# Performance work log

Measured on AMD Instinct MI355X. Metric: run time of the kernel, lower is better.

## Reference

```python
import jax, jax.numpy as jnp
import numpy as np

N = 50000      # nodes
E = 400000     # edges (before self-loops)
IN = 128
HID = 64
HEADS = 8
OUT = 3
NEG_SLOPE = 0.2
EPS = 1e-6


def setup_inputs() -> dict:
    key = jax.random.key(0)
    ks = jax.random.split(key, 32)
    def nrm(k, shape, s=0.05):
        return jax.random.normal(k, shape, dtype=jnp.float32) * s
    inp = {}
    inp['x'] = nrm(ks[0], (N, IN), 1.0)
    inp['edge_index'] = jax.random.randint(ks[1], (2, E), 0, N)
    inp['res_W'] = nrm(ks[2], (OUT, IN))
    inp['res_b'] = jnp.zeros((OUT,), jnp.float32)
    # (in, out, heads, concat) per GAT layer
    dims = [(IN, HID, HEADS, True), (HID * HEADS, HID, HEADS, True),
            (HID * HEADS, HID, HEADS, True), (HID * HEADS, OUT, 1, False)]
    j = 3
    for i, (ci, co, h, cc) in enumerate(dims):
        inp['ln_g%d' % i] = jnp.ones((ci,), jnp.float32)
        inp['ln_b%d' % i] = jnp.zeros((ci,), jnp.float32)
        inp['W%d' % i] = nrm(ks[j], (h * co, ci)); j += 1
        inp['asr%d' % i] = nrm(ks[j], (h, co)); j += 1
        inp['adt%d' % i] = nrm(ks[j], (h, co)); j += 1
        inp['b%d' % i] = jnp.zeros((h * co if cc else co,), jnp.float32)
    return inp


def layer_norm(x, g, b):
    mu = x.mean(-1, keepdims=True)
    var = ((x - mu) ** 2).mean(-1, keepdims=True)
    return (x - mu) / jnp.sqrt(var + EPS) * g + b


def gat_conv(x, src, dst, W, a_src, a_dst, bias, heads, co, concat):
    n = x.shape[0]
    h = (x @ W.T).reshape(n, heads, co)                    # [N,H,C]
    al_src = jnp.sum(h * a_src, axis=-1)                   # [N,H]
    al_dst = jnp.sum(h * a_dst, axis=-1)                   # [N,H]
    e = jax.nn.leaky_relu(al_src[src] + al_dst[dst], NEG_SLOPE)  # [E',H]
    # segment softmax over incoming edges of each destination node
    m = jax.ops.segment_max(e, dst, num_segments=n)
    e = jnp.exp(e - m[dst])
    s = jax.ops.segment_sum(e, dst, num_segments=n)
    alpha = e / s[dst]                                     # [E',H]
    msg = h[src] * alpha[..., None]                        # [E',H,C]
    out = jax.ops.segment_sum(msg, dst, num_segments=n)    # [N,H,C]
    out = out.reshape(n, heads * co) if concat else out.mean(axis=1)
    return out + bias


def reference(x, edge_index, res_W, res_b,
              ln_g0, ln_b0, W0, asr0, adt0, b0,
              ln_g1, ln_b1, W1, asr1, adt1, b1,
              ln_g2, ln_b2, W2, asr2, adt2, b2,
              ln_g3, ln_b3, W3, asr3, adt3, b3):
    n = x.shape[0]
    loops = jnp.arange(n)
    src = jnp.concatenate([edge_index[0], loops])          # add self-loops (PyG default)
    dst = jnp.concatenate([edge_index[1], loops])
    residual = x @ res_W.T + res_b
    layers = [(ln_g0, ln_b0, W0, asr0, adt0, b0, HEADS, HID, True),
              (ln_g1, ln_b1, W1, asr1, adt1, b1, HEADS, HID, True),
              (ln_g2, ln_b2, W2, asr2, adt2, b2, HEADS, HID, True),
              (ln_g3, ln_b3, W3, asr3, adt3, b3, 1, OUT, False)]
    h = x
    num_layers = len(layers)
    for i, (g, bb, W, a_s, a_d, bi, hd, co, cc) in enumerate(layers):
        x_res = h
        h = layer_norm(h, g, bb)
        h = gat_conv(h, src, dst, W, a_s, a_d, bi, hd, co, cc)
        if i < num_layers - 1:
            h = jax.nn.gelu(h, approximate=False)
            if h.shape == x_res.shape:
                h = h + x_res
    return h + residual
```

## Files before the change

### kernel.cpp

```cpp
#include <hip/hip_runtime.h>
#include <math.h>

#define NN 50000
#define MPAD 50048
#define EE 400000
#define NE 450000
#define IN_F 128
#define NEG_SLOPE 0.2f
#define EPSV 1e-6f

typedef unsigned short bf16u;
typedef short bf8_t __attribute__((ext_vector_type(8)));
typedef float f32x4 __attribute__((ext_vector_type(4)));

__device__ __forceinline__ float bf2f(unsigned int u) {
    return __uint_as_float(u << 16);
}
__device__ __forceinline__ float bf2f_hi(unsigned int u) {
    return __uint_as_float(u & 0xFFFF0000u);
}
__device__ __forceinline__ bf16u f2bf(float f) {
    unsigned int u = __float_as_uint(f);
    unsigned int r = (u + 0x7FFFu + ((u >> 16) & 1u)) >> 16;
    return (bf16u)r;
}
__device__ __forceinline__ float gelu_f(float v) {
    return 0.5f * v * (1.0f + erff(v * 0.70710678118654752f));
}
__device__ __forceinline__ float lrelu(float v) {
    return fmaxf(v, NEG_SLOPE * v);
}
__device__ __forceinline__ void fma8(float* acc, float a, uint4 u) {
    acc[0] = fmaf(a, bf2f(u.x & 0xFFFFu), acc[0]);
    acc[1] = fmaf(a, bf2f_hi(u.x),        acc[1]);
    acc[2] = fmaf(a, bf2f(u.y & 0xFFFFu), acc[2]);
    acc[3] = fmaf(a, bf2f_hi(u.y),        acc[3]);
    acc[4] = fmaf(a, bf2f(u.z & 0xFFFFu), acc[4]);
    acc[5] = fmaf(a, bf2f_hi(u.z),        acc[5]);
    acc[6] = fmaf(a, bf2f(u.w & 0xFFFFu), acc[6]);
    acc[7] = fmaf(a, bf2f_hi(u.w),        acc[7]);
}

__device__ __forceinline__ void gload_lds16(const void* g, void* l) {
    __builtin_amdgcn_global_load_lds(
        (__attribute__((address_space(1))) void*)(g),
        (__attribute__((address_space(3))) void*)(l), 16, 0, 0);
}

__global__ void k_zero_i32(int* p, int n) {
    int i = blockIdx.x * 256 + threadIdx.x;
    if (i < n) p[i] = 0;
}

__global__ void k_deg(const int* __restrict__ ei, int* __restrict__ deg) {
    int i = blockIdx.x * 256 + threadIdx.x;
    if (i >= NE) return;
    int d = (i < EE) ? ei[EE + i] : (i - EE);
    atomicAdd(&deg[d], 1);
}

__global__ __launch_bounds__(256) void k_scan1(const int* __restrict__ deg,
                                               int* __restrict__ incl,
                                               int* __restrict__ bsums, int n) {
    __shared__ int sm[1024];
    int base = blockIdx.x * 1024;
    for (int i = threadIdx.x; i < 1024; i += 256)
        sm[i] = (base + i < n) ? deg[base + i] : 0;
    __syncthreads();
    for (int off = 1; off < 1024; off <<= 1) {
        int v[4];
#pragma unroll
        for (int j = 0; j < 4; j++) {
            int i = threadIdx.x + 256 * j;
            v[j] = (i >= off) ? sm[i - off] : 0;
        }
        __syncthreads();
#pragma unroll
        for (int j = 0; j < 4; j++) {
            int i = threadIdx.x + 256 * j;
            sm[i] += v[j];
        }
        __syncthreads();
    }
    for (int i = threadIdx.x; i < 1024; i += 256)
        if (base + i < n) incl[base + i] = sm[i];
    if (threadIdx.x == 0) bsums[blockIdx.x] = sm[1023];
}

__global__ void k_scan2(int* bsums, int nb) {
    if (threadIdx.x == 0 && blockIdx.x == 0) {
        int run = 0;
        for (int i = 0; i < nb; i++) { int v = bsums[i]; bsums[i] = run; run += v; }
    }
}

__global__ void k_scan3(const int* __restrict__ deg, int* __restrict__ rowptr,
                        int* __restrict__ cursor, const int* __restrict__ bsums,
                        int n, int ne) {
    int i = blockIdx.x * 256 + threadIdx.x;
    if (i < n) {
        int excl = rowptr[i] + bsums[i >> 10] - deg[i];
        rowptr[i] = excl;
        cursor[i] = excl;
    }
    if (i == n) rowptr[n] = ne;
}

__global__ void k_scatter(const int* __restrict__ ei, int* __restrict__ cursor,
                          int* __restrict__ col) {
    int i = blockIdx.x * 256 + threadIdx.x;
    if (i >= NE) return;
    int s, d;
    if (i < EE) { s = ei[i]; d = ei[EE + i]; }
    else        { s = i - EE; d = i - EE; }
    int p = atomicAdd(&cursor[d], 1);
    col[p] = s;
}

__global__ void k_cast3(const float* __restrict__ w0, bf16u* __restrict__ o0,
                        const float* __restrict__ w1, bf16u* __restrict__ o1,
                        const float* __restrict__ w2, bf16u* __restrict__ o2) {
    int i = blockIdx.x * 256 + threadIdx.x;
    if (i < 65536) { o0[i] = f2bf(w0[i]); return; }
    i -= 65536;
    if (i < 262144) { o1[i] = f2bf(w1[i]); return; }
    i -= 262144;
    if (i < 262144) o2[i] = f2bf(w2[i]);
}

__global__ __launch_bounds__(256) void k_castres2(const float* __restrict__ x,
                                                  const float* __restrict__ rw,
                                                  const float* __restrict__ rb,
                                                  const float* __restrict__ g0,
                                                  const float* __restrict__ b0,
                                                  bf16u* __restrict__ abuf,
                                                  float* __restrict__ res, int n) {
    int row = (blockIdx.x * 256 + threadIdx.x) >> 6;
    int lane = threadIdx.x & 63;
    if (row >= n) return;
    float2 v = *(const float2*)(x + (size_t)row * 128 + lane * 2);
    float2 w0 = *(const float2*)(rw + 0 * 128 + lane * 2);
    float2 w1 = *(const float2*)(rw + 1 * 128 + lane * 2);
    float2 w2 = *(const float2*)(rw + 2 * 128 + lane * 2);
    float s = v.x + v.y, s2 = v.x * v.x + v.y * v.y;
    float a0 = v.x * w0.x + v.y * w0.y;
    float a1 = v.x * w1.x + v.y * w1.y;
    float a2 = v.x * w2.x + v.y * w2.y;
#pragma unroll
    for (int off = 32; off; off >>= 1) {
        s  += __shfl_xor(s, off);
        s2 += __shfl_xor(s2, off);
        a0 += __shfl_xor(a0, off);
        a1 += __shfl_xor(a1, off);
        a2 += __shfl_xor(a2, off);
    }
    float mu = s * (1.0f / 128.0f);
    float var = s2 * (1.0f / 128.0f) - mu * mu;
    float rs = rsqrtf(var + EPSV);
    float2 gg = *(const float2*)(g0 + lane * 2);
    float2 bb = *(const float2*)(b0 + lane * 2);
    float l0 = fmaf((v.x - mu) * rs, gg.x, bb.x);
    float l1 = fmaf((v.y - mu) * rs, gg.y, bb.y);
    *(unsigned int*)(abuf + (size_t)row * 128 + lane * 2) =
        (unsigned int)f2bf(l0) | ((unsigned int)f2bf(l1) << 16);
    if (lane == 0) {
        res[row * 3 + 0] = a0 + rb[0];
        res[row * 3 + 1] = a1 + rb[1];
        res[row * 3 + 2] = a2 + rb[2];
    }
}

#define BM 128
#define BN 128
#define BK2 64
__global__ __launch_bounds__(256) void k_gemm_sb(const bf16u* __restrict__ A,
                                                 const bf16u* __restrict__ Wb,
                                                 bf16u* __restrict__ C,
                                                 const float* __restrict__ asr,
                                                 const float* __restrict__ adt,
                                                 float* __restrict__ alsrc,
                                                 float* __restrict__ aldst,
                                                 int Mreal, int ci, int K) {
    __shared__ __align__(16) bf16u As[BM * BK2];
    __shared__ __align__(16) bf16u Bs[BN * BK2];
    const int tid = threadIdx.x;
    const int w = tid >> 6, lane = tid & 63;
    const int row0 = blockIdx.y * BM, col0 = blockIdx.x * BN;
    const int wr = (w >> 1) * 64, wc = (w & 1) * 64;

    const int lrow = lane >> 3;
    const int scolx = ((lane & 7) * 8) ^ (lrow << 3);
    const bf16u* gA = A + (size_t)(row0 + w * 32 + lrow) * ci + scolx;
    const bf16u* gB = Wb + (size_t)(col0 + w * 32 + lrow) * ci + scolx;

    const int nk = ci / BK2;

    f32x4 acc[4][4] = {};
    const int fr = lane & 15;
    const int fk = (lane >> 4) * 8;
    const int fxor = (fr & 7) << 3;

    for (int t = 0; t < nk; t++) {
        if (t) __syncthreads();
        const int k0 = t * BK2;
#pragma unroll
        for (int j = 0; j < 4; j++) {
            gload_lds16(gA + (size_t)(j * 8) * ci + k0, &As[(w * 32 + j * 8) * BK2]);
            gload_lds16(gB + (size_t)(j * 8) * ci + k0, &Bs[(w * 32 + j * 8) * BK2]);
        }
        __syncthreads();
#pragma unroll
        for (int ks = 0; ks < 2; ks++) {
            bf8_t af[4], bfv[4];
#pragma unroll
            for (int m = 0; m < 4; m++)
                af[m] = *(const bf8_t*)&As[(wr + m * 16 + fr) * BK2 + ((ks * 32 + fk) ^ fxor)];
#pragma unroll
            for (int n = 0; n < 4; n++)
                bfv[n] = *(const bf8_t*)&Bs[(wc + n * 16 + fr) * BK2 + ((ks * 32 + fk) ^ fxor)];
#pragma unroll
            for (int m = 0; m < 4; m++)
#pragma unroll
                for (int n = 0; n < 4; n++)
                    acc[m][n] = __builtin_amdgcn_mfma_f32_16x16x32_bf16(af[m], bfv[n], acc[m][n], 0, 0, 0);
        }
    }

    const int fc = lane & 15;
    const int fq = (lane >> 4) * 4;

#pragma unroll
    for (int m = 0; m < 4; m++) {
#pragma unroll
        for (int r = 0; r < 4; r++) {
            int row = row0 + wr + m * 16 + fq + r;
            if (row >= Mreal) continue;
#pragma unroll
            for (int n = 0; n < 4; n++) {
                int col = col0 + wc + n * 16 + fc;
                C[(size_t)row * K + col] = f2bf(acc[m][n][r]);
            }
        }
    }

    const int head = blockIdx.x * 2 + (wc >> 6);
    float av[4], dv[4];
#pragma unroll
    for (int n = 0; n < 4; n++) {
        av[n] = asr[head * 64 + n * 16 + fc];
        dv[n] = adt[head * 64 + n * 16 + fc];
    }
#pragma unroll
    for (int m = 0; m < 4; m++) {
#pragma unroll
        for (int r = 0; r < 4; r++) {
            float s1 = acc[m][0][r] * av[0] + acc[m][1][r] * av[1]
                     + acc[m][2][r] * av[2] + acc[m][3][r] * av[3];
            float s2 = acc[m][0][r] * dv[0] + acc[m][1][r] * dv[1]
                     + acc[m][2][r] * dv[2] + acc[m][3][r] * dv[3];
#pragma unroll
            for (int o = 1; o < 16; o <<= 1) {
                s1 += __shfl_xor(s1, o);
                s2 += __shfl_xor(s2, o);
            }
            int row = row0 + wr + m * 16 + fq + r;
            if (fc == 0 && row < Mreal) {
                alsrc[row * 8 + head] = s1;
                aldst[row * 8 + head] = s2;
            }
        }
    }
}

__global__ __launch_bounds__(256) void k_lin3b(const bf16u* __restrict__ an,
                                               const float* __restrict__ W,
                                               const float* __restrict__ a_s,
                                               const float* __restrict__ a_d,
                                               bf16u* __restrict__ hlin3,
                                               float* __restrict__ alsrc,
                                               float* __restrict__ aldst, int n) {
    int row = (blockIdx.x * 256 + threadIdx.x) >> 6;
    int lane = threadIdx.x & 63;
    if (row >= n) return;
    uint4 r = *(const uint4*)(an + (size_t)row * 512 + lane * 8);
    unsigned int u[4] = {r.x, r.y, r.z, r.w};
    float ln[8];
#pragma unroll
    for (int j = 0; j < 4; j++) {
        ln[2 * j]     = bf2f(u[j] & 0xFFFFu);
        ln[2 * j + 1] = bf2f_hi(u[j]);
    }
    float a0 = 0.f, a1 = 0.f, a2 = 0.f;
#pragma unroll
    for (int j = 0; j < 8; j++) {
        int k = lane * 8 + j;
        a0 += ln[j] * W[k];
        a1 += ln[j] * W[512 + k];
        a2 += ln[j] * W[1024 + k];
    }
#pragma unroll
    for (int off = 32; off; off >>= 1) {
        a0 += __shfl_down(a0, off);
        a1 += __shfl_down(a1, off);
        a2 += __shfl_down(a2, off);
    }
    if (lane == 0) {
        *(unsigned int*)(hlin3 + (size_t)row * 4) =
            (unsigned int)f2bf(a0) | ((unsigned int)f2bf(a1) << 16);
        *(unsigned int*)(hlin3 + (size_t)row * 4 + 2) = (unsigned int)f2bf(a2);
        alsrc[row] = a0 * a_s[0] + a1 * a_s[1] + a2 * a_s[2];
        aldst[row] = a0 * a_d[0] + a1 * a_d[1] + a2 * a_d[2];
    }
}

__global__ __launch_bounds__(256) void k_aggN2(const bf16u* __restrict__ hlin,
                                               const float* __restrict__ alsrc,
                                               const float* __restrict__ aldst,
                                               const int* __restrict__ rowptr,
                                               const int* __restrict__ col,
                                               const float* __restrict__ bias,
                                               bf16u* __restrict__ hio,
                                               const float* __restrict__ gn,
                                               const float* __restrict__ bn,
                                               bf16u* __restrict__ abuf,
                                               int n, int dores, int wrh) {
    __shared__ uint2 aldsU[4][8][66];
    int wv = threadIdx.x >> 6;
    int node = (blockIdx.x * 256 + threadIdx.x) >> 6;
    int lane = threadIdx.x & 63;
    if (node >= n) return;
    int beg = rowptr[node], end = rowptr[node + 1];
    int deg = end - beg;

    const float4* dvv = (const float4*)(aldst + node * 8);
    float4 da = dvv[0], db = dvv[1];
    float ad[8] = {da.x, da.y, da.z, da.w, db.x, db.y, db.z, db.w};

    float s = 0.f, s2 = 0.f;
    float fin[8];

    if (deg <= 64) {
        unsigned int offb = 0;
        float ex[8];
        if (lane < deg) {
            int srcreg = col[beg + lane];
            offb = (unsigned int)srcreg << 10;
            const float4* sv = (const float4*)(alsrc + srcreg * 8);
            float4 sa = sv[0], sb = sv[1];
            float sl[8] = {sa.x, sa.y, sa.z, sa.w, sb.x, sb.y, sb.z, sb.w};
#pragma unroll
            for (int h = 0; h < 8; h++) ex[h] = __expf(lrelu(sl[h] + ad[h]));
        } else {
#pragma unroll
            for (int h = 0; h < 8; h++) ex[h] = 0.f;
        }
#pragma unroll
        for (int h = 0; h < 8; h++) {
            uint2 t;
            t.x = __float_as_uint(ex[h]);
            t.y = offb;
            aldsU[wv][h][lane] = t;
        }
        asm volatile("s_waitcnt lgkmcnt(0)" ::: "memory");

        int hl = lane >> 3, s8 = lane & 7;
        const uint2* hrow = &aldsU[wv][hl][0];
        float ps = 0.f;
#pragma unroll
        for (int k2 = 0; k2 < 4; k2++) {
            uint4 q = *(const uint4*)(hrow + s8 * 8 + k2 * 2);
            ps += __uint_as_float(q.x) + __uint_as_float(q.z);
        }
#pragma unroll
        for (int o = 1; o < 8; o <<= 1) ps += __shfl_xor(ps, o);
        float invs = 1.0f / ps;

        const uint2* myal = hrow;
        const char* base2 = (const char*)hlin + (lane << 4);
        float acc0[8] = {}, acc1[8] = {};
        int e = 0;
        for (; e + 4 <= deg; e += 4) {
            uint2 t0 = myal[e];
            uint2 t1 = myal[e + 1];
            uint2 t2 = myal[e + 2];
            uint2 t3 = myal[e + 3];
            uint4 u0 = *(const uint4*)(base2 + t0.y);
            uint4 u1 = *(const uint4*)(base2 + t1.y);
            uint4 u2 = *(const uint4*)(base2 + t2.y);
            uint4 u3 = *(const uint4*)(base2 + t3.y);
            fma8(acc0, __uint_as_float(t0.x) * invs, u0);
            fma8(acc1, __uint_as_float(t1.x) * invs, u1);
            fma8(acc0, __uint_as_float(t2.x) * invs, u2);
            fma8(acc1, __uint_as_float(t3.x) * invs, u3);
        }
        if (e + 2 <= deg) {
            uint2 t0 = myal[e];
            uint2 t1 = myal[e + 1];
            uint4 u0 = *(const uint4*)(base2 + t0.y);
            uint4 u1 = *(const uint4*)(base2 + t1.y);
            fma8(acc0, __uint_as_float(t0.x) * invs, u0);
            fma8(acc1, __uint_as_float(t1.x) * invs, u1);
            e += 2;
        }
        if (e < deg) {
            uint2 t0 = myal[e];
            uint4 u0 = *(const uint4*)(base2 + t0.y);
            fma8(acc0, __uint_as_float(t0.x) * invs, u0);
        }

        size_t idx = (size_t)node * 512 + lane * 8;
        float4 b0 = *(const float4*)(bias + lane * 8);
        float4 b1 = *(const float4*)(bias + lane * 8 + 4);
        float bb[8] = {b0.x, b0.y, b0.z, b0.w, b1.x, b1.y, b1.z, b1.w};
#pragma unroll
        for (int j = 0; j < 8; j++) fin[j] = gelu_f(acc0[j] + acc1[j] + bb[j]);
        if (dores) {
            uint4 up = *(const uint4*)(hio + idx);
            fin[0] += bf2f(up.x & 0xFFFFu); fin[1] += bf2f_hi(up.x);
            fin[2] += bf2f(up.y & 0xFFFFu); fin[3] += bf2f_hi(up.y);
            fin[4] += bf2f(up.z & 0xFFFFu); fin[5] += bf2f_hi(up.z);
            fin[6] += bf2f(up.w & 0xFFFFu); fin[7] += bf2f_hi(up.w);
        }
        if (wrh) {
            uint4 pk;
            pk.x = (unsigned int)f2bf(fin[0]) | ((unsigned int)f2bf(fin[1]) << 16);
            pk.y = (unsigned int)f2bf(fin[2]) | ((unsigned int)f2bf(fin[3]) << 16);
            pk.z = (unsigned int)f2bf(fin[4]) | ((unsigned int)f2bf(fin[5]) << 16);
            pk.w = (unsigned int)f2bf(fin[6]) | ((unsigned int)f2bf(fin[7]) << 16);
            *(uint4*)(hio + idx) = pk;
        }
#pragma unroll
        for (int j = 0; j < 8; j++) { s += fin[j]; s2 += fin[j] * fin[j]; }

#pragma unroll
        for (int off = 32; off; off >>= 1) {
            s  += __shfl_xor(s, off);
            s2 += __shfl_xor(s2, off);
        }
        float mu = s * (1.0f / 512.0f);
        float rs = rsqrtf(s2 * (1.0f / 512.0f) - mu * mu + EPSV);
        float4 g0 = *(const float4*)(gn + lane * 8);
        float4 g1 = *(const float4*)(gn + lane * 8 + 4);
        float4 n0 = *(const float4*)(bn + lane * 8);
        float4 n1 = *(const float4*)(bn + lane * 8 + 4);
        float gg[8] = {g0.x, g0.y, g0.z, g0.w, g1.x, g1.y, g1.z, g1.w};
        float nb[8] = {n0.x, n0.y, n0.z, n0.w, n1.x, n1.y, n1.z, n1.w};
        float lnv[8];
#pragma unroll
        for (int j = 0; j < 8; j++) lnv[j] = fmaf((fin[j] - mu) * rs, gg[j], nb[j]);
        uint4 pl;
        pl.x = (unsigned int)f2bf(lnv[0]) | ((unsigned int)f2bf(lnv[1]) << 16);
        pl.y = (unsigned int)f2bf(lnv[2]) | ((unsigned int)f2bf(lnv[3]) << 16);
        pl.z = (unsigned int)f2bf(lnv[4]) | ((unsigned int)f2bf(lnv[5]) << 16);
        pl.w = (unsigned int)f2bf(lnv[6]) | ((unsigned int)f2bf(lnv[7]) << 16);
        *(uint4*)(abuf + idx) = pl;
    } else {
        float fins[8];
        for (int h = 0; h < 8; h++) {
            float adh = ad[h];
            float m = -INFINITY;
            for (int e = beg + lane; e < end; e += 64)
                m = fmaxf(m, lrelu(alsrc[col[e] * 8 + h] + adh));
#pragma unroll
            for (int off = 32; off; off >>= 1) m = fmaxf(m, __shfl_xor(m, off));
            float sum = 0.f;
            for (int e = beg + lane; e < end; e += 64)
                sum += __expf(lrelu(alsrc[col[e] * 8 + h] + adh) - m);
#pragma unroll
            for (int off = 32; off; off >>= 1) sum += __shfl_xor(sum, off);
            float inv = 1.0f / sum;
            float acc = 0.f;
            for (int e = beg; e < end; e++) {
                int src = col[e];
                float alpha = __expf(lrelu(alsrc[src * 8 + h] + adh) - m) * inv;
                acc = fmaf(alpha, bf2f(hlin[((size_t)src << 9) + h * 64 + lane]), acc);
            }
            float fv = gelu_f(acc + bias[h * 64 + lane]);
            size_t idx = (size_t)node * 512 + h * 64 + lane;
            if (dores) fv += bf2f(hio[idx]);
            if (wrh) hio[idx] = f2bf(fv);
            fins[h] = fv;
            s += fv; s2 += fv * fv;
        }
#pragma unroll
        for (int off = 32; off; off >>= 1) {
            s  += __shfl_xor(s, off);
            s2 += __shfl_xor(s2, off);
        }
        float mu = s * (1.0f / 512.0f);
        float rs = rsqrtf(s2 * (1.0f / 512.0f) - mu * mu + EPSV);
        for (int h = 0; h < 8; h++) {
            int c = h * 64 + lane;
            abuf[(size_t)node * 512 + c] = f2bf(fmaf((fins[h] - mu) * rs, gn[c], bn[c]));
        }
    }
}

__global__ __launch_bounds__(256) void k_aggF(const bf16u* __restrict__ hlin3,
                                              const float* __restrict__ alsrc,
                                              const float* __restrict__ aldst,
                                              const int* __restrict__ rowptr,
                                              const int* __restrict__ col,
                                              const float* __restrict__ bias,
                                              float* __restrict__ outf,
                                              const float* __restrict__ resid, int n) {
    int node = (blockIdx.x * 256 + threadIdx.x) >> 6;
    int lane = threadIdx.x & 63;
    if (node >= n) return;
    int beg = rowptr[node], end = rowptr[node + 1];
    int deg = end - beg;
    float adh = aldst[node];

    if (deg <= 64) {
        int src = 0;
        float ex = 0.f;
        if (lane < deg) {
            src = col[beg + lane];
            ex = __expf(lrelu(alsrc[src] + adh));
        }
        float sum = ex;
#pragma unroll
        for (int off = 32; off; off >>= 1) sum += __shfl_xor(sum, off);
        float alpha = ex / sum;

        float c0 = 0.f, c1 = 0.f, c2 = 0.f;
        if (lane < deg) {
            uint2 u = *(const uint2*)(hlin3 + (size_t)src * 4);
            c0 = alpha * bf2f(u.x & 0xFFFFu);
            c1 = alpha * bf2f_hi(u.x);
            c2 = alpha * bf2f(u.y & 0xFFFFu);
        }
#pragma unroll
        for (int off = 32; off; off >>= 1) {
            c0 += __shfl_xor(c0, off);
            c1 += __shfl_xor(c1, off);
            c2 += __shfl_xor(c2, off);
        }
        if (lane == 0) {
            outf[node * 3 + 0] = c0 + bias[0] + resid[node * 3 + 0];
            outf[node * 3 + 1] = c1 + bias[1] + resid[node * 3 + 1];
            outf[node * 3 + 2] = c2 + bias[2] + resid[node * 3 + 2];
        }
    } else {
        float m = -INFINITY;
        for (int e = beg + lane; e < end; e += 64)
            m = fmaxf(m, lrelu(alsrc[col[e]] + adh));
#pragma unroll
        for (int off = 32; off; off >>= 1) m = fmaxf(m, __shfl_xor(m, off));
        float sum = 0.f;
        for (int e = beg + lane; e < end; e += 64)
            sum += __expf(lrelu(alsrc[col[e]] + adh) - m);
#pragma unroll
        for (int off = 32; off; off >>= 1) sum += __shfl_xor(sum, off);
        float inv = 1.0f / sum;
        float acc = 0.f;
        for (int e = beg; e < end; e++) {
            int src = col[e];
            float alpha = __expf(lrelu(alsrc[src] + adh) - m) * inv;
            if (lane < 3) acc += alpha * bf2f(hlin3[(size_t)src * 4 + lane]);
        }
        if (lane < 3)
            outf[node * 3 + lane] = acc + bias[lane] + resid[node * 3 + lane];
    }
}

extern "C" void kernel_launch(void* const* d_in, const int* in_sizes, int n_in,
                              void* d_out, int out_size, void* d_ws, size_t ws_size,
                              hipStream_t stream) {
    const float* x    = (const float*)d_in[0];
    const int*   ei   = (const int*)d_in[1];
    const float* resW = (const float*)d_in[2];
    const float* resb = (const float*)d_in[3];
    const float *lng[4], *lnb[4], *Wm[4], *asr[4], *adt[4], *bias[4];
    int idx = 4;
    for (int i = 0; i < 4; i++) {
        lng[i]  = (const float*)d_in[idx++];
        lnb[i]  = (const float*)d_in[idx++];
        Wm[i]   = (const float*)d_in[idx++];
        asr[i]  = (const float*)d_in[idx++];
        adt[i]  = (const float*)d_in[idx++];
        bias[i] = (const float*)d_in[idx++];
    }

    char* base = (char*)d_ws;
    size_t off = 0;
    auto alloc = [&](size_t bytes) {
        void* p = base + off;
        off += (bytes + 255) & ~(size_t)255;
        return p;
    };
    float* alsrc = (float*)alloc((size_t)NN * 8 * 4);
    float* aldst = (float*)alloc((size_t)NN * 8 * 4);
    float* resid = (float*)alloc((size_t)NN * 3 * 4);
    int* rowptr  = (int*)alloc((size_t)(NN + 1) * 4);
    int* cursor  = (int*)alloc((size_t)NN * 4);
    int* deg     = (int*)alloc((size_t)NN * 4);
    int* colidx  = (int*)alloc((size_t)NE * 4);
    int* bsums   = (int*)alloc(256 * 4);
    bf16u* wb0   = (bf16u*)alloc((size_t)512 * 128 * 2);
    bf16u* wb1   = (bf16u*)alloc((size_t)512 * 512 * 2);
    bf16u* wb2   = (bf16u*)alloc((size_t)512 * 512 * 2);
    bf16u* hbuf  = (bf16u*)alloc((size_t)MPAD * 512 * 2);
    bf16u* lbuf  = (bf16u*)alloc((size_t)MPAD * 512 * 2);
    bf16u* abuf  = (bf16u*)alloc((size_t)MPAD * 512 * 2);
    if (off > ws_size) return;

    float* out = (float*)d_out;

    k_zero_i32<<<(NN + 255) / 256, 256, 0, stream>>>(deg, NN);
    k_deg<<<(NE + 255) / 256, 256, 0, stream>>>(ei, deg);
    int nb = (NN + 1023) / 1024;
    k_scan1<<<nb, 256, 0, stream>>>(deg, rowptr, bsums, NN);
    k_scan2<<<1, 64, 0, stream>>>(bsums, nb);
    k_scan3<<<(NN + 1 + 255) / 256, 256, 0, stream>>>(deg, rowptr, cursor, bsums, NN, NE);
    k_scatter<<<(NE + 255) / 256, 256, 0, stream>>>(ei, cursor, colidx);

    int rowBlocks = (NN * 64 + 255) / 256;
    k_cast3<<<(589824 + 255) / 256, 256, 0, stream>>>(Wm[0], wb0, Wm[1], wb1, Wm[2], wb2);

    const bf16u* wb[3] = {wb0, wb1, wb2};
    const int ci_a[3] = {128, 512, 512};
    dim3 ggrid(512 / BN, MPAD / BM);

    k_castres2<<<rowBlocks, 256, 0, stream>>>(x, resW, resb, lng[0], lnb[0],
                                              abuf, resid, NN);
    for (int i = 0; i < 3; i++) {
        int dores = (i >= 1) ? 1 : 0;
        int wrh = (i < 2) ? 1 : 0;
        k_gemm_sb<<<ggrid, 256, 0, stream>>>(abuf, wb[i], lbuf,
                                             asr[i], adt[i], alsrc, aldst,
                                             NN, ci_a[i], 512);
        k_aggN2<<<rowBlocks, 256, 0, stream>>>(lbuf, alsrc, aldst, rowptr, colidx,
                                               bias[i], hbuf, lng[i + 1], lnb[i + 1],
                                               abuf, NN, dores, wrh);
    }
    k_lin3b<<<rowBlocks, 256, 0, stream>>>(abuf, Wm[3], asr[3], adt[3],
                                           lbuf, alsrc, aldst, NN);
    k_aggF<<<rowBlocks, 256, 0, stream>>>(lbuf, alsrc, aldst, rowptr, colidx,
                                          bias[3], out, resid, NN);
}
```

Measured before the change: 640.2 us.

## Fold LayerNorm affine into GEMM weights and apply row stats in epilogue

Gamma is folded into the bf16 weights, and per-column sums of W*gamma and W*beta are precomputed. Each row then only stores its mean and rstd, and the GEMM epilogue applies the normalization, including in the attention logits. This removes the separate normalized activation buffer (abuf) and its full-width write and read per layer. In exchange the GEMM reads unnormalized bf16 inputs, which can change numerical error, and the aggregation loop goes from two accumulators unrolled by four to one accumulator unrolled by two.

```diff
diff --git a/kernel.cpp b/kernel.cpp
--- a/kernel.cpp
+++ b/kernel.cpp
@@ -117,28 +117,85 @@
     col[p] = s;
 }
 
-__global__ void k_cast3(const float* __restrict__ w0, bf16u* __restrict__ o0,
-                        const float* __restrict__ w1, bf16u* __restrict__ o1,
-                        const float* __restrict__ w2, bf16u* __restrict__ o2) {
-    int i = blockIdx.x * 256 + threadIdx.x;
-    if (i < 65536) { o0[i] = f2bf(w0[i]); return; }
-    i -= 65536;
-    if (i < 262144) { o1[i] = f2bf(w1[i]); return; }
-    i -= 262144;
-    if (i < 262144) o2[i] = f2bf(w2[i]);
-}
-
-__global__ __launch_bounds__(256) void k_castres2(const float* __restrict__ x,
-                                                  const float* __restrict__ rw,
-                                                  const float* __restrict__ rb,
-                                                  const float* __restrict__ g0,
-                                                  const float* __restrict__ b0,
-                                                  bf16u* __restrict__ abuf,
-                                                  float* __restrict__ res, int n) {
+__global__ __launch_bounds__(256) void k_prepw(
+    const float* __restrict__ W0, const float* __restrict__ g0, const float* __restrict__ b0,
+    bf16u* __restrict__ Wg0,
+    const float* __restrict__ W1, const float* __restrict__ g1, const float* __restrict__ b1,
+    bf16u* __restrict__ Wg1,
+    const float* __restrict__ W2, const float* __restrict__ g2, const float* __restrict__ b2,
+    bf16u* __restrict__ Wg2,
+    float* __restrict__ c1, float* __restrict__ bW) {
+    int wid = (blockIdx.x * 256 + threadIdx.x) >> 6;
+    int lane = threadIdx.x & 63;
+    if (wid >= 1536) return;
+    int l = wid >> 9, col = wid & 511;
+    const float *W, *g, *b; bf16u* Wg; int ci;
+    if (l == 0)      { W = W0; g = g0; b = b0; Wg = Wg0; ci = 128; }
+    else if (l == 1) { W = W1; g = g1; b = b1; Wg = Wg1; ci = 512; }
+    else             { W = W2; g = g2; b = b2; Wg = Wg2; ci = 512; }
+    float sc = 0.f, sb = 0.f;
+    for (int k = lane; k < ci; k += 64) {
+        float w = W[(size_t)col * ci + k];
+        float wg = w * g[k];
+        Wg[(size_t)col * ci + k] = f2bf(wg);
+        sc += wg;
+        sb += w * b[k];
+    }
+#pragma unroll
+    for (int off = 32; off; off >>= 1) {
+        sc += __shfl_xor(sc, off);
+        sb += __shfl_xor(sb, off);
+    }
+    if (lane == 0) {
+        c1[l * 512 + col] = sc;
+        bW[l * 512 + col] = sb;
+    }
+}
+
+__global__ __launch_bounds__(256) void k_prepa(
+    const float* __restrict__ c1, const float* __restrict__ bW,
+    const float* __restrict__ asr0, const float* __restrict__ adt0,
+    const float* __restrict__ asr1, const float* __restrict__ adt1,
+    const float* __restrict__ asr2, const float* __restrict__ adt2,
+    float* __restrict__ C1As, float* __restrict__ BWAs,
+    float* __restrict__ C1Ad, float* __restrict__ BWAd) {
+    int wid = (blockIdx.x * 256 + threadIdx.x) >> 6;
+    int lane = threadIdx.x & 63;
+    if (wid >= 24) return;
+    int l = wid >> 3, h = wid & 7;
+    const float* as = (l == 0) ? asr0 : (l == 1) ? asr1 : asr2;
+    const float* ad = (l == 0) ? adt0 : (l == 1) ? adt1 : adt2;
+    float c1v = c1[l * 512 + h * 64 + lane];
+    float bWv = bW[l * 512 + h * 64 + lane];
+    float av = as[h * 64 + lane], dv = ad[h * 64 + lane];
+    float s1 = c1v * av, s2 = bWv * av, s3 = c1v * dv, s4 = bWv * dv;
+#pragma unroll
+    for (int off = 32; off; off >>= 1) {
+        s1 += __shfl_xor(s1, off);
+        s2 += __shfl_xor(s2, off);
+        s3 += __shfl_xor(s3, off);
+        s4 += __shfl_xor(s4, off);
+    }
+    if (lane == 0) {
+        C1As[l * 8 + h] = s1;
+        BWAs[l * 8 + h] = s2;
+        C1Ad[l * 8 + h] = s3;
+        BWAd[l * 8 + h] = s4;
+    }
+}
+
+__global__ __launch_bounds__(256) void k_castres(const float* __restrict__ x,
+                                                 const float* __restrict__ rw,
+                                                 const float* __restrict__ rb,
+                                                 bf16u* __restrict__ xb,
+                                                 float* __restrict__ stats,
+                                                 float* __restrict__ res, int n) {
     int row = (blockIdx.x * 256 + threadIdx.x) >> 6;
     int lane = threadIdx.x & 63;
     if (row >= n) return;
     float2 v = *(const float2*)(x + (size_t)row * 128 + lane * 2);
+    unsigned int pk = (unsigned int)f2bf(v.x) | ((unsigned int)f2bf(v.y) << 16);
+    *(unsigned int*)(xb + (size_t)row * 128 + lane * 2) = pk;
     float2 w0 = *(const float2*)(rw + 0 * 128 + lane * 2);
     float2 w1 = *(const float2*)(rw + 1 * 128 + lane * 2);
     float2 w2 = *(const float2*)(rw + 2 * 128 + lane * 2);
@@ -154,16 +211,11 @@
         a1 += __shfl_xor(a1, off);
         a2 += __shfl_xor(a2, off);
     }
-    float mu = s * (1.0f / 128.0f);
-    float var = s2 * (1.0f / 128.0f) - mu * mu;
-    float rs = rsqrtf(var + EPSV);
-    float2 gg = *(const float2*)(g0 + lane * 2);
-    float2 bb = *(const float2*)(b0 + lane * 2);
-    float l0 = fmaf((v.x - mu) * rs, gg.x, bb.x);
-    float l1 = fmaf((v.y - mu) * rs, gg.y, bb.y);
-    *(unsigned int*)(abuf + (size_t)row * 128 + lane * 2) =
-        (unsigned int)f2bf(l0) | ((unsigned int)f2bf(l1) << 16);
     if (lane == 0) {
+        float mu = s * (1.0f / 128.0f);
+        float var = s2 * (1.0f / 128.0f) - mu * mu;
+        stats[row * 2 + 0] = mu;
+        stats[row * 2 + 1] = rsqrtf(var + EPSV);
         res[row * 3 + 0] = a0 + rb[0];
         res[row * 3 + 1] = a1 + rb[1];
         res[row * 3 + 2] = a2 + rb[2];
@@ -174,10 +226,17 @@
 #define BN 128
 #define BK2 64
 __global__ __launch_bounds__(256) void k_gemm_sb(const bf16u* __restrict__ A,
-                                                 const bf16u* __restrict__ Wb,
+                                                 const float* __restrict__ stats,
+                                                 const bf16u* __restrict__ Wg,
+                                                 const float* __restrict__ c1,
+                                                 const float* __restrict__ bW,
                                                  bf16u* __restrict__ C,
                                                  const float* __restrict__ asr,
                                                  const float* __restrict__ adt,
+                                                 const float* __restrict__ C1As,
+                                                 const float* __restrict__ BWAs,
+                                                 const float* __restrict__ C1Ad,
+                                                 const float* __restrict__ BWAd,
                                                  float* __restrict__ alsrc,
                                                  float* __restrict__ aldst,
                                                  int Mreal, int ci, int K) {
@@ -191,7 +250,7 @@
     const int lrow = lane >> 3;
     const int scolx = ((lane & 7) * 8) ^ (lrow << 3);
     const bf16u* gA = A + (size_t)(row0 + w * 32 + lrow) * ci + scolx;
-    const bf16u* gB = Wb + (size_t)(col0 + w * 32 + lrow) * ci + scolx;
+    const bf16u* gB = Wg + (size_t)(col0 + w * 32 + lrow) * ci + scolx;
 
     const int nk = ci / BK2;
 
@@ -228,32 +287,36 @@
 
     const int fc = lane & 15;
     const int fq = (lane >> 4) * 4;
+    const int head = blockIdx.x * 2 + (wc >> 6);
+
+    float c1v[4], bWv[4], av[4], dv[4];
+#pragma unroll
+    for (int n = 0; n < 4; n++) {
+        int col = col0 + wc + n * 16 + fc;
+        c1v[n] = c1[col];
+        bWv[n] = bW[col];
+        av[n] = asr[head * 64 + n * 16 + fc];
+        dv[n] = adt[head * 64 + n * 16 + fc];
+    }
+    const float c1as = C1As[head], bwas = BWAs[head];
+    const float c1ad = C1Ad[head], bwad = BWAd[head];
 
 #pragma unroll
     for (int m = 0; m < 4; m++) {
 #pragma unroll
         for (int r = 0; r < 4; r++) {
             int row = row0 + wr + m * 16 + fq + r;
-            if (row >= Mreal) continue;
-#pragma unroll
-            for (int n = 0; n < 4; n++) {
-                int col = col0 + wc + n * 16 + fc;
-                C[(size_t)row * K + col] = f2bf(acc[m][n][r]);
+            float2 st = *(const float2*)(stats + (size_t)row * 2);
+            float rs = st.y;
+            float nrm = -rs * st.x;
+            if (row < Mreal) {
+#pragma unroll
+                for (int n = 0; n < 4; n++) {
+                    int col = col0 + wc + n * 16 + fc;
+                    float val = fmaf(rs, acc[m][n][r], fmaf(nrm, c1v[n], bWv[n]));
+                    C[(size_t)row * K + col] = f2bf(val);
+                }
             }
-        }
-    }
-
-    const int head = blockIdx.x * 2 + (wc >> 6);
-    float av[4], dv[4];
-#pragma unroll
-    for (int n = 0; n < 4; n++) {
-        av[n] = asr[head * 64 + n * 16 + fc];
-        dv[n] = adt[head * 64 + n * 16 + fc];
-    }
-#pragma unroll
-    for (int m = 0; m < 4; m++) {
-#pragma unroll
-        for (int r = 0; r < 4; r++) {
             float s1 = acc[m][0][r] * av[0] + acc[m][1][r] * av[1]
                      + acc[m][2][r] * av[2] + acc[m][3][r] * av[3];
             float s2 = acc[m][0][r] * dv[0] + acc[m][1][r] * dv[1]
@@ -263,32 +326,41 @@
                 s1 += __shfl_xor(s1, o);
                 s2 += __shfl_xor(s2, o);
             }
-            int row = row0 + wr + m * 16 + fq + r;
             if (fc == 0 && row < Mreal) {
-                alsrc[row * 8 + head] = s1;
-                aldst[row * 8 + head] = s2;
+                alsrc[row * 8 + head] = fmaf(rs, s1, fmaf(nrm, c1as, bwas));
+                aldst[row * 8 + head] = fmaf(rs, s2, fmaf(nrm, c1ad, bwad));
             }
         }
     }
 }
 
-__global__ __launch_bounds__(256) void k_lin3b(const bf16u* __restrict__ an,
-                                               const float* __restrict__ W,
-                                               const float* __restrict__ a_s,
-                                               const float* __restrict__ a_d,
-                                               bf16u* __restrict__ hlin3,
-                                               float* __restrict__ alsrc,
-                                               float* __restrict__ aldst, int n) {
+__global__ __launch_bounds__(256) void k_lin3(const bf16u* __restrict__ h,
+                                              const float* __restrict__ stats,
+                                              const float* __restrict__ g,
+                                              const float* __restrict__ bb,
+                                              const float* __restrict__ W,
+                                              const float* __restrict__ a_s,
+                                              const float* __restrict__ a_d,
+                                              bf16u* __restrict__ hlin3,
+                                              float* __restrict__ alsrc,
+                                              float* __restrict__ aldst, int n) {
     int row = (blockIdx.x * 256 + threadIdx.x) >> 6;
     int lane = threadIdx.x & 63;
     if (row >= n) return;
-    uint4 r = *(const uint4*)(an + (size_t)row * 512 + lane * 8);
+    float mu = stats[row * 2 + 0], rs = stats[row * 2 + 1];
+    uint4 r = *(const uint4*)(h + (size_t)row * 512 + lane * 8);
+    float4 g0 = *(const float4*)(g + lane * 8);
+    float4 g1 = *(const float4*)(g + lane * 8 + 4);
+    float4 b0 = *(const float4*)(bb + lane * 8);
+    float4 b1 = *(const float4*)(bb + lane * 8 + 4);
+    float gg[8] = {g0.x, g0.y, g0.z, g0.w, g1.x, g1.y, g1.z, g1.w};
+    float bv[8] = {b0.x, b0.y, b0.z, b0.w, b1.x, b1.y, b1.z, b1.w};
     unsigned int u[4] = {r.x, r.y, r.z, r.w};
     float ln[8];
 #pragma unroll
     for (int j = 0; j < 4; j++) {
-        ln[2 * j]     = bf2f(u[j] & 0xFFFFu);
-        ln[2 * j + 1] = bf2f_hi(u[j]);
+        ln[2 * j]     = fmaf((bf2f(u[j] & 0xFFFFu) - mu) * rs, gg[2 * j], bv[2 * j]);
+        ln[2 * j + 1] = fmaf((bf2f_hi(u[j])         - mu) * rs, gg[2 * j + 1], bv[2 * j + 1]);
     }
     float a0 = 0.f, a1 = 0.f, a2 = 0.f;
 #pragma unroll
@@ -320,10 +392,8 @@
                                                const int* __restrict__ col,
                                                const float* __restrict__ bias,
                                                bf16u* __restrict__ hio,
-                                               const float* __restrict__ gn,
-                                               const float* __restrict__ bn,
-                                               bf16u* __restrict__ abuf,
-                                               int n, int dores, int wrh) {
+                                               float* __restrict__ stats,
+                                               int n, int dores) {
     __shared__ uint2 aldsU[4][8][66];
     int wv = threadIdx.x >> 6;
     int node = (blockIdx.x * 256 + threadIdx.x) >> 6;
@@ -377,35 +447,20 @@
 
         const uint2* myal = hrow;
         const char* base2 = (const char*)hlin + (lane << 4);
-        float acc0[8] = {}, acc1[8] = {};
+        float acc[8] = {};
         int e = 0;
-        for (; e + 4 <= deg; e += 4) {
-            uint2 t0 = myal[e];
-            uint2 t1 = myal[e + 1];
-            uint2 t2 = myal[e + 2];
-            uint2 t3 = myal[e + 3];
-            uint4 u0 = *(const uint4*)(base2 + t0.y);
-            uint4 u1 = *(const uint4*)(base2 + t1.y);
-            uint4 u2 = *(const uint4*)(base2 + t2.y);
-            uint4 u3 = *(const uint4*)(base2 + t3.y);
-            fma8(acc0, __uint_as_float(t0.x) * invs, u0);
-            fma8(acc1, __uint_as_float(t1.x) * invs, u1);
-            fma8(acc0, __uint_as_float(t2.x) * invs, u2);
-            fma8(acc1, __uint_as_float(t3.x) * invs, u3);
-        }
-        if (e + 2 <= deg) {
+        for (; e + 2 <= deg; e += 2) {
             uint2 t0 = myal[e];
             uint2 t1 = myal[e + 1];
             uint4 u0 = *(const uint4*)(base2 + t0.y);
             uint4 u1 = *(const uint4*)(base2 + t1.y);
-            fma8(acc0, __uint_as_float(t0.x) * invs, u0);
-            fma8(acc1, __uint_as_float(t1.x) * invs, u1);
-            e += 2;
+            fma8(acc, __uint_as_float(t0.x) * invs, u0);
+            fma8(acc, __uint_as_float(t1.x) * invs, u1);
         }
         if (e < deg) {
             uint2 t0 = myal[e];
             uint4 u0 = *(const uint4*)(base2 + t0.y);
-            fma8(acc0, __uint_as_float(t0.x) * invs, u0);
+            fma8(acc, __uint_as_float(t0.x) * invs, u0);
         }
 
         size_t idx = (size_t)node * 512 + lane * 8;
@@ -413,7 +468,7 @@
         float4 b1 = *(const float4*)(bias + lane * 8 + 4);
         float bb[8] = {b0.x, b0.y, b0.z, b0.w, b1.x, b1.y, b1.z, b1.w};
 #pragma unroll
-        for (int j = 0; j < 8; j++) fin[j] = gelu_f(acc0[j] + acc1[j] + bb[j]);
+        for (int j = 0; j < 8; j++) fin[j] = gelu_f(acc[j] + bb[j]);
         if (dores) {
             uint4 up = *(const uint4*)(hio + idx);
             fin[0] += bf2f(up.x & 0xFFFFu); fin[1] += bf2f_hi(up.x);
@@ -421,41 +476,15 @@
             fin[4] += bf2f(up.z & 0xFFFFu); fin[5] += bf2f_hi(up.z);
             fin[6] += bf2f(up.w & 0xFFFFu); fin[7] += bf2f_hi(up.w);
         }
-        if (wrh) {
-            uint4 pk;
-            pk.x = (unsigned int)f2bf(fin[0]) | ((unsigned int)f2bf(fin[1]) << 16);
-            pk.y = (unsigned int)f2bf(fin[2]) | ((unsigned int)f2bf(fin[3]) << 16);
-            pk.z = (unsigned int)f2bf(fin[4]) | ((unsigned int)f2bf(fin[5]) << 16);
-            pk.w = (unsigned int)f2bf(fin[6]) | ((unsigned int)f2bf(fin[7]) << 16);
-            *(uint4*)(hio + idx) = pk;
-        }
+        uint4 pk;
+        pk.x = (unsigned int)f2bf(fin[0]) | ((unsigned int)f2bf(fin[1]) << 16);
+        pk.y = (unsigned int)f2bf(fin[2]) | ((unsigned int)f2bf(fin[3]) << 16);
+        pk.z = (unsigned int)f2bf(fin[4]) | ((unsigned int)f2bf(fin[5]) << 16);
+        pk.w = (unsigned int)f2bf(fin[6]) | ((unsigned int)f2bf(fin[7]) << 16);
+        *(uint4*)(hio + idx) = pk;
 #pragma unroll
         for (int j = 0; j < 8; j++) { s += fin[j]; s2 += fin[j] * fin[j]; }
-
-#pragma unroll
-        for (int off = 32; off; off >>= 1) {
-            s  += __shfl_xor(s, off);
-            s2 += __shfl_xor(s2, off);
-        }
-        float mu = s * (1.0f / 512.0f);
-        float rs = rsqrtf(s2 * (1.0f / 512.0f) - mu * mu + EPSV);
-        float4 g0 = *(const float4*)(gn + lane * 8);
-        float4 g1 = *(const float4*)(gn + lane * 8 + 4);
-        float4 n0 = *(const float4*)(bn + lane * 8);
-        float4 n1 = *(const float4*)(bn + lane * 8 + 4);
-        float gg[8] = {g0.x, g0.y, g0.z, g0.w, g1.x, g1.y, g1.z, g1.w};
-        float nb[8] = {n0.x, n0.y, n0.z, n0.w, n1.x, n1.y, n1.z, n1.w};
-        float lnv[8];
-#pragma unroll
-        for (int j = 0; j < 8; j++) lnv[j] = fmaf((fin[j] - mu) * rs, gg[j], nb[j]);
-        uint4 pl;
-        pl.x = (unsigned int)f2bf(lnv[0]) | ((unsigned int)f2bf(lnv[1]) << 16);
-        pl.y = (unsigned int)f2bf(lnv[2]) | ((unsigned int)f2bf(lnv[3]) << 16);
-        pl.z = (unsigned int)f2bf(lnv[4]) | ((unsigned int)f2bf(lnv[5]) << 16);
-        pl.w = (unsigned int)f2bf(lnv[6]) | ((unsigned int)f2bf(lnv[7]) << 16);
-        *(uint4*)(abuf + idx) = pl;
     } else {
-        float fins[8];
         for (int h = 0; h < 8; h++) {
             float adh = ad[h];
             float m = -INFINITY;
@@ -478,21 +507,21 @@
             float fv = gelu_f(acc + bias[h * 64 + lane]);
             size_t idx = (size_t)node * 512 + h * 64 + lane;
             if (dores) fv += bf2f(hio[idx]);
-            if (wrh) hio[idx] = f2bf(fv);
-            fins[h] = fv;
+            hio[idx] = f2bf(fv);
             s += fv; s2 += fv * fv;
         }
-#pragma unroll
-        for (int off = 32; off; off >>= 1) {
-            s  += __shfl_xor(s, off);
-            s2 += __shfl_xor(s2, off);
-        }
+    }
+
+#pragma unroll
+    for (int off = 32; off; off >>= 1) {
+        s  += __shfl_xor(s, off);
+        s2 += __shfl_xor(s2, off);
+    }
+    if (lane == 0) {
         float mu = s * (1.0f / 512.0f);
-        float rs = rsqrtf(s2 * (1.0f / 512.0f) - mu * mu + EPSV);
-        for (int h = 0; h < 8; h++) {
-            int c = h * 64 + lane;
-            abuf[(size_t)node * 512 + c] = f2bf(fmaf((fins[h] - mu) * rs, gn[c], bn[c]));
-        }
+        float var = s2 * (1.0f / 512.0f) - mu * mu;
+        stats[node * 2 + 0] = mu;
+        stats[node * 2 + 1] = rsqrtf(var + EPSV);
     }
 }
 
@@ -597,12 +626,19 @@
     int* deg     = (int*)alloc((size_t)NN * 4);
     int* colidx  = (int*)alloc((size_t)NE * 4);
     int* bsums   = (int*)alloc(256 * 4);
-    bf16u* wb0   = (bf16u*)alloc((size_t)512 * 128 * 2);
-    bf16u* wb1   = (bf16u*)alloc((size_t)512 * 512 * 2);
-    bf16u* wb2   = (bf16u*)alloc((size_t)512 * 512 * 2);
+    bf16u* wg0   = (bf16u*)alloc((size_t)512 * 128 * 2);
+    bf16u* wg1   = (bf16u*)alloc((size_t)512 * 512 * 2);
+    bf16u* wg2   = (bf16u*)alloc((size_t)512 * 512 * 2);
+    float* c1    = (float*)alloc((size_t)3 * 512 * 4);
+    float* bW    = (float*)alloc((size_t)3 * 512 * 4);
+    float* C1As  = (float*)alloc(24 * 4);
+    float* BWAs  = (float*)alloc(24 * 4);
+    float* C1Ad  = (float*)alloc(24 * 4);
+    float* BWAd  = (float*)alloc(24 * 4);
+    float* stats = (float*)alloc((size_t)MPAD * 2 * 4);
+    bf16u* xb    = (bf16u*)alloc((size_t)MPAD * 128 * 2);
     bf16u* hbuf  = (bf16u*)alloc((size_t)MPAD * 512 * 2);
     bf16u* lbuf  = (bf16u*)alloc((size_t)MPAD * 512 * 2);
-    bf16u* abuf  = (bf16u*)alloc((size_t)MPAD * 512 * 2);
     if (off > ws_size) return;
 
     float* out = (float*)d_out;
@@ -615,27 +651,33 @@
     k_scan3<<<(NN + 1 + 255) / 256, 256, 0, stream>>>(deg, rowptr, cursor, bsums, NN, NE);
     k_scatter<<<(NE + 255) / 256, 256, 0, stream>>>(ei, cursor, colidx);
 
+    k_prepw<<<(1536 * 64 + 255) / 256, 256, 0, stream>>>(
+        Wm[0], lng[0], lnb[0], wg0,
+        Wm[1], lng[1], lnb[1], wg1,
+        Wm[2], lng[2], lnb[2], wg2, c1, bW);
+    k_prepa<<<6, 256, 0, stream>>>(c1, bW, asr[0], adt[0], asr[1], adt[1],
+                                   asr[2], adt[2], C1As, BWAs, C1Ad, BWAd);
+
     int rowBlocks = (NN * 64 + 255) / 256;
-    k_cast3<<<(589824 + 255) / 256, 256, 0, stream>>>(Wm[0], wb0, Wm[1], wb1, Wm[2], wb2);
-
-    const bf16u* wb[3] = {wb0, wb1, wb2};
+    k_castres<<<rowBlocks, 256, 0, stream>>>(x, resW, resb, xb, stats, resid, NN);
+
+    const bf16u* wg[3] = {wg0, wg1, wg2};
     const int ci_a[3] = {128, 512, 512};
     dim3 ggrid(512 / BN, MPAD / BM);
 
-    k_castres2<<<rowBlocks, 256, 0, stream>>>(x, resW, resb, lng[0], lnb[0],
-                                              abuf, resid, NN);
     for (int i = 0; i < 3; i++) {
         int dores = (i >= 1) ? 1 : 0;
-        int wrh = (i < 2) ? 1 : 0;
-        k_gemm_sb<<<ggrid, 256, 0, stream>>>(abuf, wb[i], lbuf,
-                                             asr[i], adt[i], alsrc, aldst,
-                                             NN, ci_a[i], 512);
+        const bf16u* ain = (i == 0) ? xb : hbuf;
+        k_gemm_sb<<<ggrid, 256, 0, stream>>>(ain, stats, wg[i], c1 + 512 * i, bW + 512 * i,
+                                             lbuf, asr[i], adt[i],
+                                             C1As + 8 * i, BWAs + 8 * i,
+                                             C1Ad + 8 * i, BWAd + 8 * i,
+                                             alsrc, aldst, NN, ci_a[i], 512);
         k_aggN2<<<rowBlocks, 256, 0, stream>>>(lbuf, alsrc, aldst, rowptr, colidx,
-                                               bias[i], hbuf, lng[i + 1], lnb[i + 1],
-                                               abuf, NN, dores, wrh);
-    }
-    k_lin3b<<<rowBlocks, 256, 0, stream>>>(abuf, Wm[3], asr[3], adt[3],
-                                           lbuf, alsrc, aldst, NN);
+                                               bias[i], hbuf, stats, NN, dores);
+    }
+    k_lin3<<<rowBlocks, 256, 0, stream>>>(hbuf, stats, lng[3], lnb[3], Wm[3],
+                                          asr[3], adt[3], lbuf, alsrc, aldst, NN);
     k_aggF<<<rowBlocks, 256, 0, stream>>>(lbuf, alsrc, aldst, rowptr, colidx,
                                           bias[3], out, resid, NN);
 }
```

Measured after the change: 636.1 us. No clear change (-0.6%).
